# Performance work log

Hardware: AMD Instinct MI355X
Metric: run time of the kernel (lower is better)

## Reference

```python
import jax, jax.numpy as jnp
from jax import lax
import numpy as np


def setup_inputs() -> dict:
    key = jax.random.key(0)
    k1, k2, k3 = jax.random.split(key, 3)
    B, X, Y, Z = 8, 128, 128, 128
    P = 64  # total persons across the batch
    feature = jax.random.normal(k1, (B, X, Y, Z), dtype=jnp.float32)
    # float batch indices in [0, B)
    batch_index = jnp.floor(jax.random.uniform(k2, (P,), dtype=jnp.float32) * B)
    # positions inside the voxel grid extent
    person_pos = jax.random.uniform(k3, (P, 3), dtype=jnp.float32) * jnp.array([X - 1, Y - 1, Z - 1], jnp.float32)
    min_loc_xyz = jnp.zeros((3,), jnp.float32)
    loc_delta_xyz = jnp.ones((3,), jnp.float32)
    return {"feature": feature, "batch_index": batch_index, "person_pos": person_pos,
            "min_loc_xyz": min_loc_xyz, "loc_delta_xyz": loc_delta_xyz}


def reference(feature, batch_index, person_pos, min_loc_xyz, loc_delta_xyz):
    B, X, Y, Z = feature.shape
    max_idx = jnp.array([X - 1, Y - 1, Z - 1], jnp.float32)
    # PersonPosToIndexes: world coords -> clipped voxel indices (round via +0.5 cast)
    idx = jnp.clip((person_pos - min_loc_xyz) / loc_delta_xyz, 0.0, max_idx)  # [P,3]
    full = jnp.concatenate([batch_index[:, None], idx], axis=-1)  # [P,4]
    ii = (full + 0.5).astype(jnp.int32)
    # PersonPosToHeatMap: sparse scatter of ones into dense volume
    heat = jnp.zeros(feature.shape, feature.dtype).at[ii[:, 0], ii[:, 1], ii[:, 2], ii[:, 3]].set(1.0)
    # HeatMapToWeights: 3x3x3 max-pool dilation (SAME, stride 1)
    dil = lax.reduce_window(heat, jnp.float32(-jnp.inf), lax.max,
                            (1, 3, 3, 3), (1, 1, 1, 1), 'SAME')
    nr_persons = jnp.sum(heat, axis=(1, 2, 3))  # [B]
    nr_positions = jnp.float32(X * Y * Z)
    scale_neg = (nr_persons * 27.0 / nr_positions)[:, None, None, None]
    scale_pos = (1.0 - nr_persons / nr_positions)[:, None, None, None]
    weights = (1.0 - dil) * scale_neg + heat * scale_pos
    # weighted MSE reduced per batch element, normalized by person count
    se = (feature - heat) ** 2
    loss = jnp.sum(se * weights, axis=(1, 2, 3)) / nr_persons
    return loss
```

## Files before the change

### kernel.cpp

```cpp
#include <hip/hip_runtime.h>

#define BATCH     8
#define DIM       128
#define NVOX      (BATCH * DIM * DIM * DIM)
#define NPERSON   64
#define THREADS   256
#define FLOATS_PER_BLOCK 8192
#define NBLOCK1   (NVOX / FLOATS_PER_BLOCK)
#define TSIZE     4096
#define EMPTYK    0xFFFFFFFFu
#define KEYMASK   0x00FFFFFFu
#define HEATBIT   0x40000000u

#define WS_DIL   2048
#define WS_CORR  2056
#define WS_POS   2064
#define WS_NR    2072

__global__ __launch_bounds__(THREADS) void person_loss_main(
    const float* __restrict__ feature,
    const float* __restrict__ batch_index,
    const float* __restrict__ person_pos,
    const float* __restrict__ min_loc,
    const float* __restrict__ delta,
    float* __restrict__ ws)
{
    __shared__ unsigned keys[NPERSON];
    __shared__ int      uniq[NPERSON];
    __shared__ float    lDil[BATCH], lCorr[BATCH], lPos[BATCH];
    __shared__ int      lNr[BATCH];
    __shared__ unsigned table[TSIZE];
    __shared__ float    red[4];

    const int tid  = threadIdx.x;
    const int bid  = blockIdx.x;
    const int lane = tid & 63, wave = tid >> 6;

    if (bid != 0) {
        const float4* f4 = (const float4*)feature;
        const size_t base = (size_t)(bid - 1) * (FLOATS_PER_BLOCK / 4);
        float acc = 0.f;
#pragma unroll
        for (int j = 0; j < 8; ++j) {
            float4 v = f4[base + (size_t)j * THREADS + tid];
            acc += v.x * v.x + v.y * v.y + v.z * v.z + v.w * v.w;
        }
        for (int off = 32; off > 0; off >>= 1) acc += __shfl_down(acc, off, 64);
        if (lane == 0) red[wave] = acc;
        __syncthreads();
        if (tid == 0) ws[bid - 1] = red[0] + red[1] + red[2] + red[3];
        return;
    }

    if (tid < BATCH) { lDil[tid] = 0.f; lCorr[tid] = 0.f; lPos[tid] = 0.f; lNr[tid] = 0; }
    for (int s = tid; s < TSIZE; s += THREADS) table[s] = EMPTYK;

    if (tid < NPERSON) {
        const int p = tid;
        const int b = (int)(batch_index[p] + 0.5f);
        float vx = (person_pos[p * 3 + 0] - min_loc[0]) / delta[0];
        float vy = (person_pos[p * 3 + 1] - min_loc[1]) / delta[1];
        float vz = (person_pos[p * 3 + 2] - min_loc[2]) / delta[2];
        vx = fminf(fmaxf(vx, 0.f), (float)(DIM - 1));
        vy = fminf(fmaxf(vy, 0.f), (float)(DIM - 1));
        vz = fminf(fmaxf(vz, 0.f), (float)(DIM - 1));
        const int x = (int)(vx + 0.5f);
        const int y = (int)(vy + 0.5f);
        const int z = (int)(vz + 0.5f);
        keys[p] = ((unsigned)b << 21) | ((unsigned)x << 14) | ((unsigned)y << 7) | (unsigned)z;
    }
    __syncthreads();

    if (tid < NPERSON) {
        const unsigned mykey = keys[tid];
        int u = 1;
#pragma unroll
        for (int q = 0; q < NPERSON; ++q) {
            if (q < tid && keys[q] == mykey) u = 0;
        }
        uniq[tid] = u;
        if (u) atomicAdd(&lNr[mykey >> 21], 1);
    }
    __syncthreads();

    for (int w = tid; w < NPERSON * 27; w += THREADS) {
        const int p = w / 27;
        if (!uniq[p]) continue;
        const unsigned k = keys[p];
        const int o = w % 27;
        const int x = (int)((k >> 14) & 127) + (o / 9) - 1;
        const int y = (int)((k >> 7) & 127) + ((o / 3) % 3) - 1;
        const int z = (int)(k & 127) + (o % 3) - 1;
        if ((unsigned)x > (unsigned)(DIM - 1) || (unsigned)y > (unsigned)(DIM - 1) ||
            (unsigned)z > (unsigned)(DIM - 1)) continue;
        const unsigned nk = (k & (7u << 21)) | ((unsigned)x << 14) | ((unsigned)y << 7) | (unsigned)z;
        unsigned h = ((nk * 2654435761u) >> 16) & (TSIZE - 1);
        for (;;) {
            const unsigned old = atomicCAS(&table[h], EMPTYK, nk);
            if (old == EMPTYK || (old & KEYMASK) == nk) break;
            h = (h + 1) & (TSIZE - 1);
        }
    }
    __syncthreads();

    if (tid < NPERSON && uniq[tid]) {
        const unsigned k = keys[tid];
        unsigned h = ((k * 2654435761u) >> 16) & (TSIZE - 1);
        for (;;) {
            const unsigned e = table[h];
            if (e != EMPTYK && (e & KEYMASK) == k) { atomicOr(&table[h], HEATBIT); break; }
            h = (h + 1) & (TSIZE - 1);
        }
    }
    __syncthreads();

#pragma unroll
    for (int c = 0; c < 2; ++c) {
        unsigned e[8];
#pragma unroll
        for (int j = 0; j < 8; ++j)
            e[j] = table[(c * 8 + j) * THREADS + tid];

        float f[8];
#pragma unroll
        for (int j = 0; j < 8; ++j) {
            f[j] = 0.f;
            if (e[j] != EMPTYK) {
                const unsigned k = e[j];
                const int b = (k >> 21) & 7;
                const int x = (k >> 14) & 127, y = (k >> 7) & 127, z = k & 127;
                f[j] = feature[(((size_t)b * DIM + x) * DIM + y) * DIM + z];
            }
        }
#pragma unroll
        for (int j = 0; j < 8; ++j) {
            if (e[j] == EMPTYK) continue;
            const int b = (e[j] >> 21) & 7;
            const float heat = (e[j] & HEATBIT) ? 1.f : 0.f;
            const float d = f[j] - heat;
            atomicAdd(&lDil[b], d * d);
            if (e[j] & HEATBIT) {
                atomicAdd(&lCorr[b], 1.f - 2.f * f[j]);
                const float dp = f[j] - 1.f;
                atomicAdd(&lPos[b], dp * dp);
            }
        }
    }
    __syncthreads();

    if (tid < BATCH) {
        ws[WS_DIL  + tid] = lDil[tid];
        ws[WS_CORR + tid] = lCorr[tid];
        ws[WS_POS  + tid] = lPos[tid];
        ws[WS_NR   + tid] = (float)lNr[tid];
    }
}

__global__ __launch_bounds__(THREADS) void person_loss_combine(
    const float* __restrict__ ws, float* __restrict__ out)
{
    __shared__ float red[BATCH][4];
    const int tid = threadIdx.x;
    const int lane = tid & 63, wave = tid >> 6;

    float v[BATCH];
#pragma unroll
    for (int b = 0; b < BATCH; ++b) v[b] = ws[b * (NBLOCK1 / BATCH) + tid];

#pragma unroll
    for (int b = 0; b < BATCH; ++b) {
        float s = v[b];
        for (int off = 32; off > 0; off >>= 1) s += __shfl_down(s, off, 64);
        if (lane == 0) red[b][wave] = s;
    }
    __syncthreads();

    if (tid < BATCH) {
        const int b = tid;
        const float sS2 = red[b][0] + red[b][1] + red[b][2] + red[b][3];
        const float nr  = ws[WS_NR + b];
        const float N = (float)(DIM * DIM * DIM);
        const float scale_neg = nr * 27.f / N;
        const float scale_pos = 1.f - nr / N;
        const float neg = sS2 + ws[WS_CORR + b] - ws[WS_DIL + b];
        out[b] = (scale_neg * neg + scale_pos * ws[WS_POS + b]) / nr;
    }
}

extern "C" void kernel_launch(void* const* d_in, const int* in_sizes, int n_in,
                              void* d_out, int out_size, void* d_ws, size_t ws_size,
                              hipStream_t stream)
{
    const float* feature     = (const float*)d_in[0];
    const float* batch_index = (const float*)d_in[1];
    const float* person_pos  = (const float*)d_in[2];
    const float* min_loc     = (const float*)d_in[3];
    const float* delta       = (const float*)d_in[4];
    float* out = (float*)d_out;
    float* ws  = (float*)d_ws;

    person_loss_main<<<NBLOCK1 + 1, THREADS, 0, stream>>>(
        feature, batch_index, person_pos, min_loc, delta, ws);
    person_loss_combine<<<1, THREADS, 0, stream>>>(ws, out);
}
```

Baseline: 100.1 us.

## Fuse main and combine kernels via cooperative grid sync, enlarge per-block work

Merges the dense sum-of-squares kernel and the final combine kernel into one cooperative launch that uses a grid-wide sync before block 0 does the final reduction. Each dense block now processes four times as many floats with batched float4 loads and writes per-wave partials, shrinking the grid to 513 blocks so it can be co-resident. The aim is to remove the second kernel launch and the extra workspace round trip. In exchange it adds grid-sync overhead and depends on every block being co-resident, with fewer blocks available to hide memory latency.

```diff
diff --git a/kernel.cpp b/kernel.cpp
--- a/kernel.cpp
+++ b/kernel.cpp
@@ -1,36 +1,37 @@
 #include <hip/hip_runtime.h>
+#include <hip/hip_cooperative_groups.h>
+
+namespace cg = cooperative_groups;
 
 #define BATCH     8
 #define DIM       128
 #define NVOX      (BATCH * DIM * DIM * DIM)
 #define NPERSON   64
 #define THREADS   256
-#define FLOATS_PER_BLOCK 8192
-#define NBLOCK1   (NVOX / FLOATS_PER_BLOCK)
+#define FLOATS_PER_BLOCK 32768
+#define NBLOCK_DENSE (NVOX / FLOATS_PER_BLOCK)
+#define NPARTIAL  (NBLOCK_DENSE * 4)
 #define TSIZE     4096
 #define EMPTYK    0xFFFFFFFFu
 #define KEYMASK   0x00FFFFFFu
 #define HEATBIT   0x40000000u
 
-#define WS_DIL   2048
-#define WS_CORR  2056
-#define WS_POS   2064
-#define WS_NR    2072
 
-__global__ __launch_bounds__(THREADS) void person_loss_main(
+__global__ __launch_bounds__(THREADS) void person_loss_fused(
     const float* __restrict__ feature,
     const float* __restrict__ batch_index,
     const float* __restrict__ person_pos,
     const float* __restrict__ min_loc,
     const float* __restrict__ delta,
-    float* __restrict__ ws)
+    float* __restrict__ ws,
+    float* __restrict__ out)
 {
     __shared__ unsigned keys[NPERSON];
     __shared__ int      uniq[NPERSON];
     __shared__ float    lDil[BATCH], lCorr[BATCH], lPos[BATCH];
     __shared__ int      lNr[BATCH];
     __shared__ unsigned table[TSIZE];
-    __shared__ float    red[4];
+    __shared__ float    sums[BATCH];
 
     const int tid  = threadIdx.x;
     const int bid  = blockIdx.x;
@@ -41,149 +42,137 @@
         const size_t base = (size_t)(bid - 1) * (FLOATS_PER_BLOCK / 4);
         float acc = 0.f;
 #pragma unroll
-        for (int j = 0; j < 8; ++j) {
-            float4 v = f4[base + (size_t)j * THREADS + tid];
-            acc += v.x * v.x + v.y * v.y + v.z * v.z + v.w * v.w;
+        for (int c = 0; c < 4; ++c) {
+            float4 v[8];
+#pragma unroll
+            for (int j = 0; j < 8; ++j)
+                v[j] = f4[base + (size_t)(c * 8 + j) * THREADS + tid];
+#pragma unroll
+            for (int j = 0; j < 8; ++j)
+                acc += v[j].x * v[j].x + v[j].y * v[j].y
+                     + v[j].z * v[j].z + v[j].w * v[j].w;
         }
         for (int off = 32; off > 0; off >>= 1) acc += __shfl_down(acc, off, 64);
-        if (lane == 0) red[wave] = acc;
+        if (lane == 0) ws[(bid - 1) * 4 + wave] = acc;
+    } else {
+        if (tid < BATCH) { lDil[tid] = 0.f; lCorr[tid] = 0.f; lPos[tid] = 0.f; lNr[tid] = 0; }
+        for (int s = tid; s < TSIZE; s += THREADS) table[s] = EMPTYK;
+
+        if (tid < NPERSON) {
+            const int p = tid;
+            const int b = (int)(batch_index[p] + 0.5f);
+            float vx = (person_pos[p * 3 + 0] - min_loc[0]) / delta[0];
+            float vy = (person_pos[p * 3 + 1] - min_loc[1]) / delta[1];
+            float vz = (person_pos[p * 3 + 2] - min_loc[2]) / delta[2];
+            vx = fminf(fmaxf(vx, 0.f), (float)(DIM - 1));
+            vy = fminf(fmaxf(vy, 0.f), (float)(DIM - 1));
+            vz = fminf(fmaxf(vz, 0.f), (float)(DIM - 1));
+            const int x = (int)(vx + 0.5f);
+            const int y = (int)(vy + 0.5f);
+            const int z = (int)(vz + 0.5f);
+            keys[p] = ((unsigned)b << 21) | ((unsigned)x << 14) | ((unsigned)y << 7) | (unsigned)z;
+        }
         __syncthreads();
-        if (tid == 0) ws[bid - 1] = red[0] + red[1] + red[2] + red[3];
-        return;
+
+        if (tid < NPERSON) {
+            const unsigned mykey = keys[tid];
+            int u = 1;
+#pragma unroll
+            for (int q = 0; q < NPERSON; ++q) {
+                if (q < tid && keys[q] == mykey) u = 0;
+            }
+            uniq[tid] = u;
+            if (u) atomicAdd(&lNr[mykey >> 21], 1);
+        }
+        __syncthreads();
+
+        for (int w = tid; w < NPERSON * 27; w += THREADS) {
+            const int p = w / 27;
+            if (!uniq[p]) continue;
+            const unsigned k = keys[p];
+            const int o = w % 27;
+            const int x = (int)((k >> 14) & 127) + (o / 9) - 1;
+            const int y = (int)((k >> 7) & 127) + ((o / 3) % 3) - 1;
+            const int z = (int)(k & 127) + (o % 3) - 1;
+            if ((unsigned)x > (unsigned)(DIM - 1) || (unsigned)y > (unsigned)(DIM - 1) ||
+                (unsigned)z > (unsigned)(DIM - 1)) continue;
+            const unsigned nk = (k & (7u << 21)) | ((unsigned)x << 14) | ((unsigned)y << 7) | (unsigned)z;
+            unsigned h = ((nk * 2654435761u) >> 16) & (TSIZE - 1);
+            for (;;) {
+                const unsigned old = atomicCAS(&table[h], EMPTYK, nk);
+                if (old == EMPTYK || (old & KEYMASK) == nk) break;
+                h = (h + 1) & (TSIZE - 1);
+            }
+        }
+        __syncthreads();
+
+        if (tid < NPERSON && uniq[tid]) {
+            const unsigned k = keys[tid];
+            unsigned h = ((k * 2654435761u) >> 16) & (TSIZE - 1);
+            for (;;) {
+                const unsigned e = table[h];
+                if (e != EMPTYK && (e & KEYMASK) == k) { atomicOr(&table[h], HEATBIT); break; }
+                h = (h + 1) & (TSIZE - 1);
+            }
+        }
+        __syncthreads();
+
+#pragma unroll
+        for (int c = 0; c < 2; ++c) {
+            unsigned e[8];
+#pragma unroll
+            for (int j = 0; j < 8; ++j)
+                e[j] = table[(c * 8 + j) * THREADS + tid];
+
+            float f[8];
+#pragma unroll
+            for (int j = 0; j < 8; ++j) {
+                f[j] = 0.f;
+                if (e[j] != EMPTYK) {
+                    const unsigned k = e[j];
+                    const int b = (k >> 21) & 7;
+                    const int x = (k >> 14) & 127, y = (k >> 7) & 127, z = k & 127;
+                    f[j] = feature[(((size_t)b * DIM + x) * DIM + y) * DIM + z];
+                }
+            }
+#pragma unroll
+            for (int j = 0; j < 8; ++j) {
+                if (e[j] == EMPTYK) continue;
+                const int b = (e[j] >> 21) & 7;
+                const float heat = (e[j] & HEATBIT) ? 1.f : 0.f;
+                const float d = f[j] - heat;
+                atomicAdd(&lDil[b], d * d);
+                if (e[j] & HEATBIT) {
+                    atomicAdd(&lCorr[b], 1.f - 2.f * f[j]);
+                    const float dp = f[j] - 1.f;
+                    atomicAdd(&lPos[b], dp * dp);
+                }
+            }
+        }
+        __syncthreads();
     }
 
-    if (tid < BATCH) { lDil[tid] = 0.f; lCorr[tid] = 0.f; lPos[tid] = 0.f; lNr[tid] = 0; }
-    for (int s = tid; s < TSIZE; s += THREADS) table[s] = EMPTYK;
+    __threadfence();
+    cg::this_grid().sync();
 
-    if (tid < NPERSON) {
-        const int p = tid;
-        const int b = (int)(batch_index[p] + 0.5f);
-        float vx = (person_pos[p * 3 + 0] - min_loc[0]) / delta[0];
-        float vy = (person_pos[p * 3 + 1] - min_loc[1]) / delta[1];
-        float vz = (person_pos[p * 3 + 2] - min_loc[2]) / delta[2];
-        vx = fminf(fmaxf(vx, 0.f), (float)(DIM - 1));
-        vy = fminf(fmaxf(vy, 0.f), (float)(DIM - 1));
-        vz = fminf(fmaxf(vz, 0.f), (float)(DIM - 1));
-        const int x = (int)(vx + 0.5f);
-        const int y = (int)(vy + 0.5f);
-        const int z = (int)(vz + 0.5f);
-        keys[p] = ((unsigned)b << 21) | ((unsigned)x << 14) | ((unsigned)y << 7) | (unsigned)z;
-    }
-    __syncthreads();
+    if (bid == 0) {
+        const float4* w4 = (const float4*)ws;
+        const float4 a = w4[2 * tid];
+        const float4 b = w4[2 * tid + 1];
+        float s = a.x + a.y + a.z + a.w + b.x + b.y + b.z + b.w;
+        for (int off = 16; off > 0; off >>= 1) s += __shfl_down(s, off, 32);
+        if ((tid & 31) == 0) sums[tid >> 5] = s;
+        __syncthreads();
 
-    if (tid < NPERSON) {
-        const unsigned mykey = keys[tid];
-        int u = 1;
-#pragma unroll
-        for (int q = 0; q < NPERSON; ++q) {
-            if (q < tid && keys[q] == mykey) u = 0;
+        if (tid < BATCH) {
+            const float sS2 = sums[tid];
+            const float nr  = (float)lNr[tid];
+            const float N   = (float)(DIM * DIM * DIM);
+            const float scale_neg = nr * 27.f / N;
+            const float scale_pos = 1.f - nr / N;
+            const float neg = sS2 + lCorr[tid] - lDil[tid];
+            out[tid] = (scale_neg * neg + scale_pos * lPos[tid]) / nr;
         }
-        uniq[tid] = u;
-        if (u) atomicAdd(&lNr[mykey >> 21], 1);
-    }
-    __syncthreads();
-
-    for (int w = tid; w < NPERSON * 27; w += THREADS) {
-        const int p = w / 27;
-        if (!uniq[p]) continue;
-        const unsigned k = keys[p];
-        const int o = w % 27;
-        const int x = (int)((k >> 14) & 127) + (o / 9) - 1;
-        const int y = (int)((k >> 7) & 127) + ((o / 3) % 3) - 1;
-        const int z = (int)(k & 127) + (o % 3) - 1;
-        if ((unsigned)x > (unsigned)(DIM - 1) || (unsigned)y > (unsigned)(DIM - 1) ||
-            (unsigned)z > (unsigned)(DIM - 1)) continue;
-        const unsigned nk = (k & (7u << 21)) | ((unsigned)x << 14) | ((unsigned)y << 7) | (unsigned)z;
-        unsigned h = ((nk * 2654435761u) >> 16) & (TSIZE - 1);
-        for (;;) {
-            const unsigned old = atomicCAS(&table[h], EMPTYK, nk);
-            if (old == EMPTYK || (old & KEYMASK) == nk) break;
-            h = (h + 1) & (TSIZE - 1);
-        }
-    }
-    __syncthreads();
-
-    if (tid < NPERSON && uniq[tid]) {
-        const unsigned k = keys[tid];
-        unsigned h = ((k * 2654435761u) >> 16) & (TSIZE - 1);
-        for (;;) {
-            const unsigned e = table[h];
-            if (e != EMPTYK && (e & KEYMASK) == k) { atomicOr(&table[h], HEATBIT); break; }
-            h = (h + 1) & (TSIZE - 1);
-        }
-    }
-    __syncthreads();
-
-#pragma unroll
-    for (int c = 0; c < 2; ++c) {
-        unsigned e[8];
-#pragma unroll
-        for (int j = 0; j < 8; ++j)
-            e[j] = table[(c * 8 + j) * THREADS + tid];
-
-        float f[8];
-#pragma unroll
-        for (int j = 0; j < 8; ++j) {
-            f[j] = 0.f;
-            if (e[j] != EMPTYK) {
-                const unsigned k = e[j];
-                const int b = (k >> 21) & 7;
-                const int x = (k >> 14) & 127, y = (k >> 7) & 127, z = k & 127;
-                f[j] = feature[(((size_t)b * DIM + x) * DIM + y) * DIM + z];
-            }
-        }
-#pragma unroll
-        for (int j = 0; j < 8; ++j) {
-            if (e[j] == EMPTYK) continue;
-            const int b = (e[j] >> 21) & 7;
-            const float heat = (e[j] & HEATBIT) ? 1.f : 0.f;
-            const float d = f[j] - heat;
-            atomicAdd(&lDil[b], d * d);
-            if (e[j] & HEATBIT) {
-                atomicAdd(&lCorr[b], 1.f - 2.f * f[j]);
-                const float dp = f[j] - 1.f;
-                atomicAdd(&lPos[b], dp * dp);
-            }
-        }
-    }
-    __syncthreads();
-
-    if (tid < BATCH) {
-        ws[WS_DIL  + tid] = lDil[tid];
-        ws[WS_CORR + tid] = lCorr[tid];
-        ws[WS_POS  + tid] = lPos[tid];
-        ws[WS_NR   + tid] = (float)lNr[tid];
-    }
-}
-
-__global__ __launch_bounds__(THREADS) void person_loss_combine(
-    const float* __restrict__ ws, float* __restrict__ out)
-{
-    __shared__ float red[BATCH][4];
-    const int tid = threadIdx.x;
-    const int lane = tid & 63, wave = tid >> 6;
-
-    float v[BATCH];
-#pragma unroll
-    for (int b = 0; b < BATCH; ++b) v[b] = ws[b * (NBLOCK1 / BATCH) + tid];
-
-#pragma unroll
-    for (int b = 0; b < BATCH; ++b) {
-        float s = v[b];
-        for (int off = 32; off > 0; off >>= 1) s += __shfl_down(s, off, 64);
-        if (lane == 0) red[b][wave] = s;
-    }
-    __syncthreads();
-
-    if (tid < BATCH) {
-        const int b = tid;
-        const float sS2 = red[b][0] + red[b][1] + red[b][2] + red[b][3];
-        const float nr  = ws[WS_NR + b];
-        const float N = (float)(DIM * DIM * DIM);
-        const float scale_neg = nr * 27.f / N;
-        const float scale_pos = 1.f - nr / N;
-        const float neg = sS2 + ws[WS_CORR + b] - ws[WS_DIL + b];
-        out[b] = (scale_neg * neg + scale_pos * ws[WS_POS + b]) / nr;
     }
 }
 
@@ -199,7 +188,8 @@
     float* out = (float*)d_out;
     float* ws  = (float*)d_ws;
 
-    person_loss_main<<<NBLOCK1 + 1, THREADS, 0, stream>>>(
-        feature, batch_index, person_pos, min_loc, delta, ws);
-    person_loss_combine<<<1, THREADS, 0, stream>>>(ws, out);
+    void* args[] = { &feature, &batch_index, &person_pos, &min_loc, &delta, &ws, &out };
+    hipLaunchCooperativeKernel(person_loss_fused,
+                               dim3(NBLOCK_DENSE + 1), dim3(THREADS),
+                               args, 0, stream);
 }
```

Result: slower. 223.0 us (+122.8%).
